# Performance work log

Measured on AMD Instinct MI355X. Metric: run time of the kernel, lower is better.

The kernel has to match this reference:

```python
import jax, jax.numpy as jnp
import numpy as np

NB_HEAD = 8
SIZE_PER_HEAD = 64
EMB = 512  # word embedding dim; output_dim = NB_HEAD*SIZE_PER_HEAD = 512
B, S = 8, 4096


def setup_inputs() -> dict:
    key = jax.random.key(0)
    ks = jax.random.split(key, 8)
    return {
        "Q_seq": jax.random.normal(ks[0], (B, S, EMB), dtype=jnp.float32),
        "K_seq": jax.random.normal(ks[1], (B, S, EMB), dtype=jnp.float32),
        "V_seq": jax.random.normal(ks[2], (B, S, EMB), dtype=jnp.float32),
        "Q_len": jax.random.randint(ks[3], (B, 1), 0, S, dtype=jnp.int32),
        "V_len": jax.random.randint(ks[4], (B, 1), 0, SIZE_PER_HEAD, dtype=jnp.int32),
        "WQ": jax.random.normal(ks[5], (EMB, NB_HEAD * SIZE_PER_HEAD), dtype=jnp.float32),
        "WK": jax.random.normal(ks[6], (EMB, NB_HEAD * SIZE_PER_HEAD), dtype=jnp.float32),
        "WV": jax.random.normal(ks[7], (EMB, NB_HEAD * SIZE_PER_HEAD), dtype=jnp.float32),
    }


def _proj_heads(x, W):
    # [B,S,E] @ [E,H*d] -> [B,H,S,d]
    y = jnp.einsum('bse,eo->bso', x, W)
    y = y.reshape(y.shape[0], y.shape[1], NB_HEAD, SIZE_PER_HEAD)
    return jnp.transpose(y, (0, 2, 1, 3))


def reference(Q_seq, K_seq, V_seq, Q_len, V_len, WQ, WK, WV):
    H, d = NB_HEAD, SIZE_PER_HEAD
    Q = _proj_heads(Q_seq, WQ)  # [B,H,S,d]
    K = _proj_heads(K_seq, WK)
    V = _proj_heads(V_seq, WV)

    A = (Q * K) / jnp.asarray(d, Q.dtype) ** 0.5  # elementwise, [B,H,S,d]

    # TF code transposes A to [B,d,S,H] and masks along axis 1 (size d) using
    # V_len, then transposes back. Equivalent: additive mask on the LAST axis.
    vmask = jax.nn.one_hot(V_len[:, 0], d, dtype=A.dtype)       # [B,d]
    vmask = 1.0 - jnp.cumsum(vmask, axis=1)                      # [B,d]
    A = A - (1.0 - vmask)[:, None, None, :] * 1e12

    A = jax.nn.softmax(A, axis=-1)  # softmax over d (last axis), as tf.nn.softmax

    O = A * V                              # [B,H,S,d]
    O = jnp.transpose(O, (0, 2, 1, 3))     # [B,S,H,d]
    O = O.reshape(O.shape[0], O.shape[1], H * d)  # [B,S,H*d]

    # multiplicative mask over sequence axis using Q_len
    qmask = jax.nn.one_hot(Q_len[:, 0], O.shape[1], dtype=O.dtype)  # [B,S]
    qmask = 1.0 - jnp.cumsum(qmask, axis=1)
    return O * qmask[:, :, None]
```

## Files before the change

kernel.cpp:

```cpp
#include <hip/hip_runtime.h>
#include <hip/hip_bf16.h>

typedef unsigned short u16;
typedef unsigned int   u32;
typedef _Float16 f16;
typedef _Float16 f16x8 __attribute__((ext_vector_type(8)));
typedef float    f32x4 __attribute__((ext_vector_type(4)));
typedef float    f32x8 __attribute__((ext_vector_type(8)));

#define BATCH 8
#define SEQ   4096
#define EMB   512
#define NCOL  512

__device__ __forceinline__ void gll16(const void* g, void* l) {
  __builtin_amdgcn_global_load_lds((__attribute__((address_space(1))) void*)g,
                                   (__attribute__((address_space(3))) void*)l,
                                   16, 0, 0);
}

__global__ __launch_bounds__(256) void prep_w(
    const float* __restrict__ Wq, const float* __restrict__ Wk,
    const float* __restrict__ Wv, u16* __restrict__ out)
{
  __shared__ u16 tile[64][65];
  const int z = blockIdx.z;
  const float* in = (z < 2) ? Wq : (z < 4) ? Wk : Wv;
  const bool lo = (z == 1 || z == 3);
  u16* o = out + (size_t)z * EMB * NCOL;
  const int r0 = blockIdx.y * 64, c0 = blockIdx.x * 64;
  const int tx = threadIdx.x, ty = threadIdx.y;
#pragma unroll
  for (int i = 0; i < 16; ++i) {
    const int r = ty * 16 + i;
    const float x = in[(size_t)(r0 + r) * NCOL + (c0 + tx)];
    const f16 h = (f16)x;
    const f16 v = lo ? (f16)((x - (float)h) * 256.0f) : h;
    tile[r][tx] = __builtin_bit_cast(u16, v);
  }
  __syncthreads();
#pragma unroll
  for (int i = 0; i < 16; ++i) {
    const int rr = ty * 16 + i;
    o[(size_t)(c0 + rr) * EMB + (r0 + tx)] = tile[tx][rr];
  }
}

__global__ __launch_bounds__(256, 2) void fused_attn(
    const float* __restrict__ Xq, const float* __restrict__ Xk,
    const float* __restrict__ Xv,
    const int* __restrict__ Qlen, const int* __restrict__ Vlen,
    const u16* __restrict__ Wt,
    float* __restrict__ out)
{
  const int b  = blockIdx.z;
  const int s0 = blockIdx.x * 64;
  const int c0 = blockIdx.y * 128;
  const int qlen = Qlen[b];
  const int t = threadIdx.x;

  if (s0 >= qlen) {
    const f32x4 z4 = {0.f, 0.f, 0.f, 0.f};
#pragma unroll
    for (int it = 0; it < 8; ++it) {
      const int f4  = it * 256 + t;
      const int row = f4 >> 5;
      const int col = (f4 & 31) * 4;
      *(f32x4*)(out + (size_t)(b * SEQ + s0 + row) * NCOL + c0 + col) = z4;
    }
    return;
  }
  const int vlen = Vlen[b];
  const int vl = (vlen == 0) ? 64 : vlen;

  __shared__ unsigned char smem[65536] __attribute__((aligned(16)));
  float* Xq_s  = (float*)(smem);
  float* Xk_s  = (float*)(smem + 8192);
  float* Xv_s  = (float*)(smem + 16384);
  u16*   Wqh_s = (u16*)(smem + 24576);
  u16*   Wql_s = (u16*)(smem + 32768);
  u16*   Wkh_s = (u16*)(smem + 40960);
  u16*   Wkl_s = (u16*)(smem + 49152);
  u16*   Wv_s  = (u16*)(smem + 57344);

  const u16* Wqh_g = Wt;
  const u16* Wql_g = Wt + 1 * EMB * NCOL;
  const u16* Wkh_g = Wt + 2 * EMB * NCOL;
  const u16* Wkl_g = Wt + 3 * EMB * NCOL;
  const u16* Wv_g  = Wt + 4 * EMB * NCOL;

  f32x4 accQ[2][4], accQc[2][4], accK[2][4], accKc[2][4], accV[2][4];
#pragma unroll
  for (int rt = 0; rt < 2; ++rt)
#pragma unroll
    for (int ct = 0; ct < 4; ++ct) {
      const f32x4 z = {0.f, 0.f, 0.f, 0.f};
      accQ[rt][ct] = z; accQc[rt][ct] = z;
      accK[rt][ct] = z; accKc[rt][ct] = z;
      accV[rt][ct] = z;
    }

  const int w    = t >> 6;
  const int lane = t & 63;
  const int quad = lane >> 4;
  const int l15  = lane & 15;
  const int wr   = w >> 1;
  const int wc   = w & 1;

  const int xrow = t >> 3;
  const int k4   = (t & 7) * 4;
  const size_t xg = (size_t)(b * SEQ + s0 + xrow) * EMB + k4;
  const int wn   = t >> 2;
  const int k8   = (t & 3) * 8;
  const int wg   = (c0 + wn) * EMB + k8;
  const int xl   = t * 4;
  const int wlo  = t * 8;

  for (int kk = 0; kk < EMB; kk += 32) {
    __syncthreads();
    gll16(Xq + xg + kk,             Xq_s + xl);
    gll16(Xq + xg + 32 * EMB + kk,  Xq_s + 1024 + xl);
    gll16(Xk + xg + kk,             Xk_s + xl);
    gll16(Xk + xg + 32 * EMB + kk,  Xk_s + 1024 + xl);
    gll16(Xv + xg + kk,             Xv_s + xl);
    gll16(Xv + xg + 32 * EMB + kk,  Xv_s + 1024 + xl);
    gll16(Wqh_g + wg + kk,            Wqh_s + wlo);
    gll16(Wqh_g + wg + 64 * EMB + kk, Wqh_s + 2048 + wlo);
    gll16(Wql_g + wg + kk,            Wql_s + wlo);
    gll16(Wql_g + wg + 64 * EMB + kk, Wql_s + 2048 + wlo);
    gll16(Wkh_g + wg + kk,            Wkh_s + wlo);
    gll16(Wkh_g + wg + 64 * EMB + kk, Wkh_s + 2048 + wlo);
    gll16(Wkl_g + wg + kk,            Wkl_s + wlo);
    gll16(Wkl_g + wg + 64 * EMB + kk, Wkl_s + 2048 + wlo);
    gll16(Wv_g + wg + kk,             Wv_s + wlo);
    gll16(Wv_g + wg + 64 * EMB + kk,  Wv_s + 2048 + wlo);
    __syncthreads();

    f16x8 aqh[2], aql[2], akh[2], akl[2], av[2];
#pragma unroll
    for (int rt = 0; rt < 2; ++rt) {
      const int ao = (wr * 32 + rt * 16 + l15) * 32 + quad * 8;
      const f32x8 xq = *(const f32x8*)(Xq_s + ao);
      const f32x8 xk = *(const f32x8*)(Xk_s + ao);
      const f32x8 xv = *(const f32x8*)(Xv_s + ao);
#pragma unroll
      for (int j = 0; j < 8; ++j) {
        const float q = xq[j];
        const f16 qh = (f16)q;
        aqh[rt][j] = qh;
        aql[rt][j] = (f16)((q - (float)qh) * 256.0f);
        const float k = xk[j];
        const f16 kh = (f16)k;
        akh[rt][j] = kh;
        akl[rt][j] = (f16)((k - (float)kh) * 256.0f);
        av[rt][j]  = (f16)xv[j];
      }
    }
#pragma unroll
    for (int ct = 0; ct < 4; ++ct) {
      const int bo = (wc * 64 + ct * 16 + l15) * 32 + quad * 8;
      const f16x8 bqh = *(const f16x8*)(Wqh_s + bo);
      const f16x8 bql = *(const f16x8*)(Wql_s + bo);
      const f16x8 bkh = *(const f16x8*)(Wkh_s + bo);
      const f16x8 bkl = *(const f16x8*)(Wkl_s + bo);
      const f16x8 bv  = *(const f16x8*)(Wv_s  + bo);
#pragma unroll
      for (int rt = 0; rt < 2; ++rt) {
        accQ [rt][ct] = __builtin_amdgcn_mfma_f32_16x16x32_f16(aqh[rt], bqh, accQ [rt][ct], 0, 0, 0);
        accQc[rt][ct] = __builtin_amdgcn_mfma_f32_16x16x32_f16(aqh[rt], bql, accQc[rt][ct], 0, 0, 0);
        accQc[rt][ct] = __builtin_amdgcn_mfma_f32_16x16x32_f16(aql[rt], bqh, accQc[rt][ct], 0, 0, 0);
        accK [rt][ct] = __builtin_amdgcn_mfma_f32_16x16x32_f16(akh[rt], bkh, accK [rt][ct], 0, 0, 0);
        accKc[rt][ct] = __builtin_amdgcn_mfma_f32_16x16x32_f16(akh[rt], bkl, accKc[rt][ct], 0, 0, 0);
        accKc[rt][ct] = __builtin_amdgcn_mfma_f32_16x16x32_f16(akl[rt], bkh, accKc[rt][ct], 0, 0, 0);
        accV [rt][ct] = __builtin_amdgcn_mfma_f32_16x16x32_f16(av[rt],  bv,  accV [rt][ct], 0, 0, 0);
      }
    }
  }

  const float scale = 0.125f;
  const float rs    = 1.0f / 256.0f;
#pragma unroll
  for (int rt = 0; rt < 2; ++rt) {
#pragma unroll
    for (int r = 0; r < 4; ++r) {
      const int s = s0 + wr * 32 + rt * 16 + quad * 4 + r;
      const float qm = (s < qlen) ? 1.0f : 0.0f;
      float a[4]; bool msk[4];
      float mx = -3.0e38f;
#pragma unroll
      for (int ct = 0; ct < 4; ++ct) {
        const float q = accQ[rt][ct][r] + accQc[rt][ct][r] * rs;
        const float k = accK[rt][ct][r] + accKc[rt][ct][r] * rs;
        const float v = q * k * scale;
        a[ct] = v;
        msk[ct] = (ct * 16 + l15) < vl;
        if (msk[ct]) mx = fmaxf(mx, v);
      }
#pragma unroll
      for (int off = 1; off < 16; off <<= 1) mx = fmaxf(mx, __shfl_xor(mx, off));
      float e[4], sum = 0.f;
#pragma unroll
      for (int ct = 0; ct < 4; ++ct) {
        e[ct] = msk[ct] ? __expf(a[ct] - mx) : 0.0f;
        sum += e[ct];
      }
#pragma unroll
      for (int off = 1; off < 16; off <<= 1) sum += __shfl_xor(sum, off);
      const float inv = qm / sum;
      const size_t ob = (size_t)(b * SEQ + s) * NCOL + c0 + wc * 64 + l15;
#pragma unroll
      for (int ct = 0; ct < 4; ++ct) {
        out[ob + ct * 16] = e[ct] * inv * accV[rt][ct][r];
      }
    }
  }
}

extern "C" void kernel_launch(void* const* d_in, const int* in_sizes, int n_in,
                              void* d_out, int out_size, void* d_ws, size_t ws_size,
                              hipStream_t stream) {
  const float* Xq   = (const float*)d_in[0];
  const float* Xk   = (const float*)d_in[1];
  const float* Xv   = (const float*)d_in[2];
  const int*   Qlen = (const int*)d_in[3];
  const int*   Vlen = (const int*)d_in[4];
  const float* Wq   = (const float*)d_in[5];
  const float* Wk   = (const float*)d_in[6];
  const float* Wv   = (const float*)d_in[7];
  u16*   Wt  = (u16*)d_ws;
  float* out = (float*)d_out;

  dim3 pg(8, 8, 5), pb(64, 4, 1);
  prep_w<<<pg, pb, 0, stream>>>(Wq, Wk, Wv, Wt);

  dim3 g(SEQ / 64, NCOL / 128, BATCH), blk(256, 1, 1);
  fused_attn<<<g, blk, 0, stream>>>(Xq, Xk, Xv, Qlen, Vlen, Wt, out);
}
```

Before: 334.0 us.

## Restructure fused attention: 512-thread blocks, staged fp16 split X, direct weight loads

Blocks now cover 64 rows by 256 columns with 8 waves. Each wave owns 32 columns, and the head softmax is split across wave pairs, combined through LDS max/sum exchange. X is loaded into registers, converted once to hi/lo fp16 planes, and double-buffered in padded LDS, so the split is no longer recomputed per wave. Weight fragments are read directly from global/L2 instead of being staged in LDS. This halves X reloads across column blocks and overlaps global loads with MFMA, at the cost of uncoalesced weight reads from global memory and higher register pressure.

```diff
diff --git a/kernel.cpp b/kernel.cpp
--- a/kernel.cpp
+++ b/kernel.cpp
@@ -1,23 +1,15 @@
 #include <hip/hip_runtime.h>
-#include <hip/hip_bf16.h>
 
 typedef unsigned short u16;
-typedef unsigned int   u32;
 typedef _Float16 f16;
+typedef _Float16 f16x4 __attribute__((ext_vector_type(4)));
 typedef _Float16 f16x8 __attribute__((ext_vector_type(8)));
 typedef float    f32x4 __attribute__((ext_vector_type(4)));
-typedef float    f32x8 __attribute__((ext_vector_type(8)));
 
 #define BATCH 8
 #define SEQ   4096
 #define EMB   512
 #define NCOL  512
-
-__device__ __forceinline__ void gll16(const void* g, void* l) {
-  __builtin_amdgcn_global_load_lds((__attribute__((address_space(1))) void*)g,
-                                   (__attribute__((address_space(3))) void*)l,
-                                   16, 0, 0);
-}
 
 __global__ __launch_bounds__(256) void prep_w(
     const float* __restrict__ Wq, const float* __restrict__ Wk,
@@ -46,7 +38,11 @@
   }
 }
 
-__global__ __launch_bounds__(256, 2) void fused_attn(
+#define PSTRIDE 40
+#define PLANE   (64*PSTRIDE)
+#define BUFSZ   (5*PLANE)
+
+__global__ __launch_bounds__(512, 4) void fused_attn(
     const float* __restrict__ Xq, const float* __restrict__ Xk,
     const float* __restrict__ Xv,
     const int* __restrict__ Qlen, const int* __restrict__ Vlen,
@@ -55,7 +51,7 @@
 {
   const int b  = blockIdx.z;
   const int s0 = blockIdx.x * 64;
-  const int c0 = blockIdx.y * 128;
+  const int c0 = blockIdx.y * 256;
   const int qlen = Qlen[b];
   const int t = threadIdx.x;
 
@@ -63,9 +59,9 @@
     const f32x4 z4 = {0.f, 0.f, 0.f, 0.f};
 #pragma unroll
     for (int it = 0; it < 8; ++it) {
-      const int f4  = it * 256 + t;
-      const int row = f4 >> 5;
-      const int col = (f4 & 31) * 4;
+      const int f4  = it * 512 + t;
+      const int row = f4 >> 6;
+      const int col = (f4 & 63) * 4;
       *(f32x4*)(out + (size_t)(b * SEQ + s0 + row) * NCOL + c0 + col) = z4;
     }
     return;
@@ -73,145 +69,177 @@
   const int vlen = Vlen[b];
   const int vl = (vlen == 0) ? 64 : vlen;
 
-  __shared__ unsigned char smem[65536] __attribute__((aligned(16)));
-  float* Xq_s  = (float*)(smem);
-  float* Xk_s  = (float*)(smem + 8192);
-  float* Xv_s  = (float*)(smem + 16384);
-  u16*   Wqh_s = (u16*)(smem + 24576);
-  u16*   Wql_s = (u16*)(smem + 32768);
-  u16*   Wkh_s = (u16*)(smem + 40960);
-  u16*   Wkl_s = (u16*)(smem + 49152);
-  u16*   Wv_s  = (u16*)(smem + 57344);
-
-  const u16* Wqh_g = Wt;
-  const u16* Wql_g = Wt + 1 * EMB * NCOL;
-  const u16* Wkh_g = Wt + 2 * EMB * NCOL;
-  const u16* Wkl_g = Wt + 3 * EMB * NCOL;
-  const u16* Wv_g  = Wt + 4 * EMB * NCOL;
-
-  f32x4 accQ[2][4], accQc[2][4], accK[2][4], accKc[2][4], accV[2][4];
-#pragma unroll
-  for (int rt = 0; rt < 2; ++rt)
-#pragma unroll
-    for (int ct = 0; ct < 4; ++ct) {
+  __shared__ f16 smem[2 * BUFSZ] __attribute__((aligned(16)));
+
+  const int w    = t >> 6;
+  const int lane = t & 63;
+  const int quad = lane >> 4;
+  const int l15  = lane & 15;
+
+  const int    srow = t >> 3;
+  const int    sk4  = (t & 7) * 4;
+  const size_t xg   = (size_t)(b * SEQ + s0 + srow) * EMB + sk4;
+  const int    swo  = srow * PSTRIDE + sk4;
+
+  const size_t wb = (size_t)(c0 + w * 32 + l15) * EMB + quad * 8;
+  const u16* Wqh_g = Wt                + wb;
+  const u16* Wql_g = Wt + 1 * EMB*NCOL + wb;
+  const u16* Wkh_g = Wt + 2 * EMB*NCOL + wb;
+  const u16* Wkl_g = Wt + 3 * EMB*NCOL + wb;
+  const u16* Wv_g  = Wt + 4 * EMB*NCOL + wb;
+
+  const int ao = l15 * PSTRIDE + quad * 8;
+
+  f32x4 accQ[4][2], accQc[4][2], accK[4][2], accKc[4][2], accV[4][2];
+#pragma unroll
+  for (int rt = 0; rt < 4; ++rt)
+#pragma unroll
+    for (int ct = 0; ct < 2; ++ct) {
       const f32x4 z = {0.f, 0.f, 0.f, 0.f};
       accQ[rt][ct] = z; accQc[rt][ct] = z;
       accK[rt][ct] = z; accKc[rt][ct] = z;
       accV[rt][ct] = z;
     }
 
-  const int w    = t >> 6;
-  const int lane = t & 63;
-  const int quad = lane >> 4;
-  const int l15  = lane & 15;
-  const int wr   = w >> 1;
-  const int wc   = w & 1;
-
-  const int xrow = t >> 3;
-  const int k4   = (t & 7) * 4;
-  const size_t xg = (size_t)(b * SEQ + s0 + xrow) * EMB + k4;
-  const int wn   = t >> 2;
-  const int k8   = (t & 3) * 8;
-  const int wg   = (c0 + wn) * EMB + k8;
-  const int xl   = t * 4;
-  const int wlo  = t * 8;
-
-  for (int kk = 0; kk < EMB; kk += 32) {
+  f32x4 rq[2], rk[2], rv[2];
+
+#define LOADX(SLOT, TT) do { \
+    rq[SLOT] = *(const f32x4*)(Xq + xg + (TT) * 32); \
+    rk[SLOT] = *(const f32x4*)(Xk + xg + (TT) * 32); \
+    rv[SLOT] = *(const f32x4*)(Xv + xg + (TT) * 32); \
+  } while (0)
+
+#define STAGE(SLOT, BOFS) do { \
+    f16* p_ = smem + (BOFS); \
+    f16x4 qh_, ql_, kh_, kl_, vh_; \
+    _Pragma("unroll") \
+    for (int j = 0; j < 4; ++j) { \
+      const float xq_ = rq[SLOT][j]; const f16 qhh_ = (f16)xq_; \
+      qh_[j] = qhh_; ql_[j] = (f16)((xq_ - (float)qhh_) * 256.0f); \
+      const float xk_ = rk[SLOT][j]; const f16 khh_ = (f16)xk_; \
+      kh_[j] = khh_; kl_[j] = (f16)((xk_ - (float)khh_) * 256.0f); \
+      vh_[j] = (f16)rv[SLOT][j]; \
+    } \
+    *(f16x4*)(p_ + 0 * PLANE + swo) = qh_; \
+    *(f16x4*)(p_ + 1 * PLANE + swo) = ql_; \
+    *(f16x4*)(p_ + 2 * PLANE + swo) = kh_; \
+    *(f16x4*)(p_ + 3 * PLANE + swo) = kl_; \
+    *(f16x4*)(p_ + 4 * PLANE + swo) = vh_; \
+  } while (0)
+
+#define COMPUTE(BOFS, KK) do { \
+    const f16* p_ = smem + (BOFS); \
+    const int kk_ = (KK); \
+    f16x8 bqh_[2], bql_[2], bkh_[2], bkl_[2], bv_[2]; \
+    _Pragma("unroll") \
+    for (int ct = 0; ct < 2; ++ct) { \
+      const size_t wo_ = (size_t)ct * 16 * EMB + kk_; \
+      bqh_[ct] = *(const f16x8*)(Wqh_g + wo_); \
+      bql_[ct] = *(const f16x8*)(Wql_g + wo_); \
+      bkh_[ct] = *(const f16x8*)(Wkh_g + wo_); \
+      bkl_[ct] = *(const f16x8*)(Wkl_g + wo_); \
+      bv_ [ct] = *(const f16x8*)(Wv_g  + wo_); \
+    } \
+    _Pragma("unroll") \
+    for (int rt = 0; rt < 4; ++rt) { \
+      const int ao_ = ao + rt * 16 * PSTRIDE; \
+      const f16x8 aqh_ = *(const f16x8*)(p_ + 0 * PLANE + ao_); \
+      const f16x8 aql_ = *(const f16x8*)(p_ + 1 * PLANE + ao_); \
+      const f16x8 akh_ = *(const f16x8*)(p_ + 2 * PLANE + ao_); \
+      const f16x8 akl_ = *(const f16x8*)(p_ + 3 * PLANE + ao_); \
+      const f16x8 av_  = *(const f16x8*)(p_ + 4 * PLANE + ao_); \
+      _Pragma("unroll") \
+      for (int ct = 0; ct < 2; ++ct) { \
+        accQ [rt][ct] = __builtin_amdgcn_mfma_f32_16x16x32_f16(aqh_, bqh_[ct], accQ [rt][ct], 0, 0, 0); \
+        accQc[rt][ct] = __builtin_amdgcn_mfma_f32_16x16x32_f16(aqh_, bql_[ct], accQc[rt][ct], 0, 0, 0); \
+        accQc[rt][ct] = __builtin_amdgcn_mfma_f32_16x16x32_f16(aql_, bqh_[ct], accQc[rt][ct], 0, 0, 0); \
+        accK [rt][ct] = __builtin_amdgcn_mfma_f32_16x16x32_f16(akh_, bkh_[ct], accK [rt][ct], 0, 0, 0); \
+        accKc[rt][ct] = __builtin_amdgcn_mfma_f32_16x16x32_f16(akh_, bkl_[ct], accKc[rt][ct], 0, 0, 0); \
+        accKc[rt][ct] = __builtin_amdgcn_mfma_f32_16x16x32_f16(akl_, bkh_[ct], accKc[rt][ct], 0, 0, 0); \
+        accV [rt][ct] = __builtin_amdgcn_mfma_f32_16x16x32_f16(av_,  bv_[ct],  accV [rt][ct], 0, 0, 0); \
+      } \
+    } \
+  } while (0)
+
+  LOADX(0, 0);
+  LOADX(1, 1);
+  STAGE(0, 0);
+  __syncthreads();
+
+#pragma unroll 1
+  for (int tt = 0; tt < 16; tt += 2) {
+    STAGE(1, BUFSZ);
+    if (tt < 14) LOADX(0, tt + 2);
+    COMPUTE(0, tt * 32);
     __syncthreads();
-    gll16(Xq + xg + kk,             Xq_s + xl);
-    gll16(Xq + xg + 32 * EMB + kk,  Xq_s + 1024 + xl);
-    gll16(Xk + xg + kk,             Xk_s + xl);
-    gll16(Xk + xg + 32 * EMB + kk,  Xk_s + 1024 + xl);
-    gll16(Xv + xg + kk,             Xv_s + xl);
-    gll16(Xv + xg + 32 * EMB + kk,  Xv_s + 1024 + xl);
-    gll16(Wqh_g + wg + kk,            Wqh_s + wlo);
-    gll16(Wqh_g + wg + 64 * EMB + kk, Wqh_s + 2048 + wlo);
-    gll16(Wql_g + wg + kk,            Wql_s + wlo);
-    gll16(Wql_g + wg + 64 * EMB + kk, Wql_s + 2048 + wlo);
-    gll16(Wkh_g + wg + kk,            Wkh_s + wlo);
-    gll16(Wkh_g + wg + 64 * EMB + kk, Wkh_s + 2048 + wlo);
-    gll16(Wkl_g + wg + kk,            Wkl_s + wlo);
-    gll16(Wkl_g + wg + 64 * EMB + kk, Wkl_s + 2048 + wlo);
-    gll16(Wv_g + wg + kk,             Wv_s + wlo);
-    gll16(Wv_g + wg + 64 * EMB + kk,  Wv_s + 2048 + wlo);
+    if (tt < 14) STAGE(0, 0);
+    if (tt < 13) LOADX(1, tt + 3);
+    COMPUTE(BUFSZ, (tt + 1) * 32);
     __syncthreads();
-
-    f16x8 aqh[2], aql[2], akh[2], akl[2], av[2];
-#pragma unroll
-    for (int rt = 0; rt < 2; ++rt) {
-      const int ao = (wr * 32 + rt * 16 + l15) * 32 + quad * 8;
-      const f32x8 xq = *(const f32x8*)(Xq_s + ao);
-      const f32x8 xk = *(const f32x8*)(Xk_s + ao);
-      const f32x8 xv = *(const f32x8*)(Xv_s + ao);
-#pragma unroll
-      for (int j = 0; j < 8; ++j) {
-        const float q = xq[j];
-        const f16 qh = (f16)q;
-        aqh[rt][j] = qh;
-        aql[rt][j] = (f16)((q - (float)qh) * 256.0f);
-        const float k = xk[j];
-        const f16 kh = (f16)k;
-        akh[rt][j] = kh;
-        akl[rt][j] = (f16)((k - (float)kh) * 256.0f);
-        av[rt][j]  = (f16)xv[j];
-      }
-    }
-#pragma unroll
-    for (int ct = 0; ct < 4; ++ct) {
-      const int bo = (wc * 64 + ct * 16 + l15) * 32 + quad * 8;
-      const f16x8 bqh = *(const f16x8*)(Wqh_s + bo);
-      const f16x8 bql = *(const f16x8*)(Wql_s + bo);
-      const f16x8 bkh = *(const f16x8*)(Wkh_s + bo);
-      const f16x8 bkl = *(const f16x8*)(Wkl_s + bo);
-      const f16x8 bv  = *(const f16x8*)(Wv_s  + bo);
-#pragma unroll
-      for (int rt = 0; rt < 2; ++rt) {
-        accQ [rt][ct] = __builtin_amdgcn_mfma_f32_16x16x32_f16(aqh[rt], bqh, accQ [rt][ct], 0, 0, 0);
-        accQc[rt][ct] = __builtin_amdgcn_mfma_f32_16x16x32_f16(aqh[rt], bql, accQc[rt][ct], 0, 0, 0);
-        accQc[rt][ct] = __builtin_amdgcn_mfma_f32_16x16x32_f16(aql[rt], bqh, accQc[rt][ct], 0, 0, 0);
-        accK [rt][ct] = __builtin_amdgcn_mfma_f32_16x16x32_f16(akh[rt], bkh, accK [rt][ct], 0, 0, 0);
-        accKc[rt][ct] = __builtin_amdgcn_mfma_f32_16x16x32_f16(akh[rt], bkl, accKc[rt][ct], 0, 0, 0);
-        accKc[rt][ct] = __builtin_amdgcn_mfma_f32_16x16x32_f16(akl[rt], bkh, accKc[rt][ct], 0, 0, 0);
-        accV [rt][ct] = __builtin_amdgcn_mfma_f32_16x16x32_f16(av[rt],  bv,  accV [rt][ct], 0, 0, 0);
-      }
-    }
-  }
+  }
+
+#undef LOADX
+#undef STAGE
+#undef COMPUTE
 
   const float scale = 0.125f;
   const float rs    = 1.0f / 256.0f;
-#pragma unroll
-  for (int rt = 0; rt < 2; ++rt) {
+  float* smf = (float*)smem;
+
+  float eA[4][2][4];
+  float lm[4][4], lsum[4][4];
+
+#pragma unroll
+  for (int rt = 0; rt < 4; ++rt) {
 #pragma unroll
     for (int r = 0; r < 4; ++r) {
-      const int s = s0 + wr * 32 + rt * 16 + quad * 4 + r;
-      const float qm = (s < qlen) ? 1.0f : 0.0f;
-      float a[4]; bool msk[4];
+      float a[2]; bool msk[2];
       float mx = -3.0e38f;
 #pragma unroll
-      for (int ct = 0; ct < 4; ++ct) {
+      for (int ct = 0; ct < 2; ++ct) {
         const float q = accQ[rt][ct][r] + accQc[rt][ct][r] * rs;
         const float k = accK[rt][ct][r] + accKc[rt][ct][r] * rs;
-        const float v = q * k * scale;
-        a[ct] = v;
-        msk[ct] = (ct * 16 + l15) < vl;
-        if (msk[ct]) mx = fmaxf(mx, v);
+        a[ct] = q * k * scale;
+        msk[ct] = ((w & 1) * 32 + ct * 16 + l15) < vl;
+        if (msk[ct]) mx = fmaxf(mx, a[ct]);
       }
 #pragma unroll
       for (int off = 1; off < 16; off <<= 1) mx = fmaxf(mx, __shfl_xor(mx, off));
-      float e[4], sum = 0.f;
-#pragma unroll
-      for (int ct = 0; ct < 4; ++ct) {
-        e[ct] = msk[ct] ? __expf(a[ct] - mx) : 0.0f;
-        sum += e[ct];
+      float sum = 0.f;
+#pragma unroll
+      for (int ct = 0; ct < 2; ++ct) {
+        const float e = msk[ct] ? __expf(a[ct] - mx) : 0.0f;
+        eA[rt][ct][r] = e;
+        sum += e;
       }
 #pragma unroll
       for (int off = 1; off < 16; off <<= 1) sum += __shfl_xor(sum, off);
-      const float inv = qm / sum;
-      const size_t ob = (size_t)(b * SEQ + s) * NCOL + c0 + wc * 64 + l15;
-#pragma unroll
-      for (int ct = 0; ct < 4; ++ct) {
-        out[ob + ct * 16] = e[ct] * inv * accV[rt][ct][r];
+      lm[rt][r] = mx; lsum[rt][r] = sum;
+      const int row = rt * 16 + quad * 4 + r;
+      if (l15 == 0) {
+        smf[(w * 64 + row) * 2 + 0] = mx;
+        smf[(w * 64 + row) * 2 + 1] = sum;
       }
+    }
+  }
+  __syncthreads();
+
+#pragma unroll
+  for (int rt = 0; rt < 4; ++rt) {
+#pragma unroll
+    for (int r = 0; r < 4; ++r) {
+      const int row = rt * 16 + quad * 4 + r;
+      const int s   = s0 + row;
+      const float pm = smf[((w ^ 1) * 64 + row) * 2 + 0];
+      const float ps = smf[((w ^ 1) * 64 + row) * 2 + 1];
+      const float m  = lm[rt][r];
+      const float M  = fmaxf(m, pm);
+      const float S  = lsum[rt][r] * __expf(m - M) + ps * __expf(pm - M);
+      const float qm = (s < qlen) ? 1.0f : 0.0f;
+      const float f  = __expf(m - M) * qm / S;
+      const size_t ob = (size_t)(b * SEQ + s) * NCOL + c0 + w * 32 + l15;
+      out[ob]      = eA[rt][0][r] * f * accV[rt][0][r];
+      out[ob + 16] = eA[rt][1][r] * f * accV[rt][1][r];
     }
   }
 }
@@ -233,6 +261,6 @@
   dim3 pg(8, 8, 5), pb(64, 4, 1);
   prep_w<<<pg, pb, 0, stream>>>(Wq, Wk, Wv, Wt);
 
-  dim3 g(SEQ / 64, NCOL / 128, BATCH), blk(256, 1, 1);
+  dim3 g(SEQ / 64, NCOL / 256, BATCH), blk(512, 1, 1);
   fused_attn<<<g, blk, 0, stream>>>(Xq, Xk, Xv, Qlen, Vlen, Wt, out);
 }
```

New measurement: 1.227 ms. +267.3%, slower.
